# Optimization experiments

Measured on AMD Instinct MI355X. Metric: run time of the kernel, lower is better.

## Reference

```python
import jax, jax.numpy as jnp
import numpy as np

B, S, E = 1, 2048, 2048
H, KVH, D = 16, 4, 128  # query heads, kv heads, head dim (emb_kq == emb_v == 128)
SPLITS = (H * D, KVH * D, KVH * D)  # fused qkv output split sizes


def _rope_tables(seq_len, dim, base=10000.0):
    inv_freq = 1.0 / (base ** (jnp.arange(0, dim, 2, dtype=jnp.float32) / dim))
    t = jnp.arange(seq_len, dtype=jnp.float32)
    freqs = jnp.outer(t, inv_freq)  # [S, D/2]
    emb = jnp.concatenate([freqs, freqs], axis=-1)  # [S, D]
    return jnp.cos(emb), jnp.sin(emb)


def _rotate_half(x):
    x1, x2 = jnp.split(x, 2, axis=-1)
    return jnp.concatenate([-x2, x1], axis=-1)


def _apply_rope(x, cos, sin):
    # x: [B, S, h, D]; cos/sin: [S, D]
    c = cos[None, :, None, :]
    s = sin[None, :, None, :]
    return x * c + _rotate_half(x) * s


def setup_inputs() -> dict:
    key = jax.random.key(0)
    k1, k2, k3 = jax.random.split(key, 3)
    x = jax.random.normal(k1, (B, S, E), dtype=jnp.float32)
    w_qkv = jax.random.normal(k2, (sum(SPLITS), E), dtype=jnp.float32) * 0.02
    w_dense = jax.random.normal(k3, (E, H * D), dtype=jnp.float32) * 0.02
    return {"x": x, "w_qkv": w_qkv, "w_dense": w_dense}


def reference(x, w_qkv, w_dense):
    # fused QKV projection: [B, S, sum(SPLITS)]
    qkv = jnp.einsum("bse,fe->bsf", x, w_qkv)
    q, k, v = jnp.split(qkv, np.cumsum(SPLITS)[:-1].tolist(), axis=-1)
    q = q.reshape(B, S, H, D)
    k = k.reshape(B, S, KVH, D)
    v = v.reshape(B, S, KVH, D)

    # rotary position encoding on q, k
    cos, sin = _rope_tables(S, D)
    q = _apply_rope(q, cos, sin)
    k = _apply_rope(k, cos, sin)

    # GQA: expand kv heads to match query heads
    rep = H // KVH
    k = jnp.repeat(k, rep, axis=2)  # [B, S, H, D]
    v = jnp.repeat(v, rep, axis=2)

    # SDPA, causal
    scale = 1.0 / jnp.sqrt(jnp.asarray(D, dtype=x.dtype))
    scores = jnp.einsum("bqhd,bkhd->bhqk", q, k) * scale
    causal = jnp.tril(jnp.ones((S, S), dtype=bool))
    scores = jnp.where(causal[None, None], scores, jnp.asarray(-jnp.inf, scores.dtype))
    attn = jax.nn.softmax(scores, axis=-1)
    ctx = jnp.einsum("bhqk,bkhd->bqhd", attn, v).reshape(B, S, H * D)

    # output projection
    return jnp.einsum("bsf,ef->bse", ctx, w_dense)
```

## Files before the change

### kernel.cpp

```cpp
#include <hip/hip_runtime.h>
#include <hip/hip_bf16.h>
#include <math.h>

typedef __bf16 bf16;
typedef __bf16 bf16x4 __attribute__((ext_vector_type(4)));
typedef __bf16 bf16x8 __attribute__((ext_vector_type(8)));
typedef float  f32x4  __attribute__((ext_vector_type(4)));
typedef float  f32x16 __attribute__((ext_vector_type(16)));

#define S_LEN 2048
#define EMB   2048
#define NH    16
#define NKV   4
#define HD    128
#define FQKV  3072

__device__ __forceinline__ f32x4 mfma16(bf16x8 a, bf16x8 b, f32x4 c) {
  return __builtin_amdgcn_mfma_f32_16x16x32_bf16(a, b, c, 0, 0, 0);
}
__device__ __forceinline__ f32x16 mfma32(bf16x8 a, bf16x8 b, f32x16 c) {
  return __builtin_amdgcn_mfma_f32_32x32x16_bf16(a, b, c, 0, 0, 0);
}
__device__ __forceinline__ f32x16 zero16() {
  f32x16 v;
#pragma unroll
  for (int i = 0; i < 16; ++i) v[i] = 0.f;
  return v;
}

__global__ void rope_init(float2* __restrict__ rt) {
  const int idx = blockIdx.x * blockDim.x + threadIdx.x;
  const int spos = idx >> 6, f = idx & 63;
  const float inv = exp2f(-(float)f * (13.287712379549449f / 64.0f));
  float s, c;
  sincosf((float)spos * inv, &s, &c);
  rt[idx] = make_float2(c, s);
}

__global__ void cvt3_kernel(const float* __restrict__ a, bf16* __restrict__ ab, int na4,
                            const float* __restrict__ b, bf16* __restrict__ bb, int nb4,
                            const float* __restrict__ c, bf16* __restrict__ cb, int nc4) {
  int i = blockIdx.x * blockDim.x + threadIdx.x;
  const int stride = gridDim.x * blockDim.x;
  const int total = na4 + nb4 + nc4;
  for (; i < total; i += stride) {
    const float* src; bf16* dst; int j = i;
    if (j < na4)            { src = a; dst = ab; }
    else if (j < na4 + nb4) { j -= na4; src = b; dst = bb; }
    else                    { j -= na4 + nb4; src = c; dst = cb; }
    float4 v = reinterpret_cast<const float4*>(src)[j];
    bf16x4 o;
    o[0] = (bf16)v.x; o[1] = (bf16)v.y; o[2] = (bf16)v.z; o[3] = (bf16)v.w;
    reinterpret_cast<bf16x4*>(dst)[j] = o;
  }
}

template<int BN>
__global__ __launch_bounds__(256, 2) void gemm_bt(
    const bf16* __restrict__ A, const bf16* __restrict__ B,
    int M, int N, int K, int mode,
    bf16* __restrict__ qb, bf16* __restrict__ kb, bf16* __restrict__ vtb,
    float* __restrict__ outf, const float2* __restrict__ rt)
{
  constexpr int NFR = BN / 16;
  __shared__ __align__(16) bf16 As[128 * 64];
  __shared__ __align__(16) bf16 Bs[BN * 64];
  const int tid = threadIdx.x;
  const int w  = tid >> 6;
  const int l  = tid & 63;
  const int li = l & 15, lh = l >> 4;
  const int m0 = blockIdx.y * 128, n0 = blockIdx.x * BN;

  f32x4 acc[2][NFR];
#pragma unroll
  for (int i = 0; i < 2; ++i)
#pragma unroll
    for (int j = 0; j < NFR; ++j) acc[i][j] = f32x4{0.f, 0.f, 0.f, 0.f};

  const int srow = l >> 3;
  const int schk = l & 7;

  for (int k0 = 0; k0 < K; k0 += 64) {
#pragma unroll
    for (int i = 0; i < 4; ++i) {
      const int row = i * 32 + w * 8 + srow;
      const int sch = schk ^ (row & 7);
      const bf16* ga = A + (size_t)(m0 + row) * K + (k0 + sch * 8);
      bf16* la = As + (i * 32 + w * 8) * 64;
      __builtin_amdgcn_global_load_lds((const __attribute__((address_space(1))) void*)ga,
                                       (__attribute__((address_space(3))) void*)la, 16, 0, 0);
    }
#pragma unroll
    for (int i = 0; i < BN / 32; ++i) {
      const int row = i * 32 + w * 8 + srow;
      const int sch = schk ^ (row & 7);
      const bf16* gb = B + (size_t)(n0 + row) * K + (k0 + sch * 8);
      bf16* lb = Bs + (i * 32 + w * 8) * 64;
      __builtin_amdgcn_global_load_lds((const __attribute__((address_space(1))) void*)gb,
                                       (__attribute__((address_space(3))) void*)lb, 16, 0, 0);
    }
    __syncthreads();
#pragma unroll
    for (int kc = 0; kc < 2; ++kc) {
      bf16x8 afr[2], bfr[NFR];
#pragma unroll
      for (int mt = 0; mt < 2; ++mt) {
        const int mr = w * 32 + mt * 16 + li;
        const int c  = (kc * 4 + lh) ^ (mr & 7);
        afr[mt] = *reinterpret_cast<const bf16x8*>((const char*)As + mr * 128 + c * 16);
      }
#pragma unroll
      for (int nt = 0; nt < NFR; ++nt) {
        const int nr = nt * 16 + li;
        const int c  = (kc * 4 + lh) ^ (nr & 7);
        bfr[nt] = *reinterpret_cast<const bf16x8*>((const char*)Bs + nr * 128 + c * 16);
      }
#pragma unroll
      for (int nt = 0; nt < NFR; ++nt) {
        acc[0][nt] = mfma16(afr[0], bfr[nt], acc[0][nt]);
        acc[1][nt] = mfma16(afr[1], bfr[nt], acc[1][nt]);
      }
    }
    __syncthreads();
  }

  const int row_base = m0 + w * 32;
  if (BN == 64 || mode == 1) {
#pragma unroll
    for (int mt = 0; mt < 2; ++mt)
#pragma unroll
      for (int nt = 0; nt < NFR; ++nt)
#pragma unroll
        for (int r = 0; r < 4; ++r) {
          const int sr = row_base + mt * 16 + lh * 4 + r;
          const int sc = n0 + nt * 16 + li;
          outf[(size_t)sr * N + sc] = acc[mt][nt][r];
        }
  } else {
    if constexpr (BN == 128) {
      int seg, hh;
      if (n0 < NH * HD)             { seg = 0; hh = n0 >> 7; }
      else if (n0 < (NH + NKV) * HD){ seg = 1; hh = (n0 - NH * HD) >> 7; }
      else                          { seg = 2; hh = (n0 - (NH + NKV) * HD) >> 7; }

      const int T = row_base >> 5;
      if (seg == 2) {
        bf16* vdst = vtb + (size_t)hh * S_LEN * HD + (size_t)T * 4096;
#pragma unroll
        for (int mt = 0; mt < 2; ++mt) {
          const int qp = mt * 4 + lh;
          const int jj = (qp >> 2) & 1, hiv = qp & 1, ebase = 4 * ((qp >> 1) & 1);
#pragma unroll
          for (int nt = 0; nt < 8; ++nt) {
            const int dt = nt >> 1;
            const int lqv = (nt & 1) * 16 + li;
            bf16x4 pk;
#pragma unroll
            for (int r = 0; r < 4; ++r) pk[r] = (bf16)acc[mt][nt][r];
            *reinterpret_cast<bf16x4*>(
                vdst + ((dt * 2 + jj) * 2 + hiv) * 256 + lqv * 8 + ebase) = pk;
          }
        }
      } else {
        bf16* dst = ((seg == 0) ? (qb + (size_t)hh * S_LEN * HD)
                                : (kb + (size_t)hh * S_LEN * HD)) + (size_t)T * 4096;
        const float qscale = (seg == 0) ? 0.08838834764831845f : 1.0f;
        const int hi2 = li >> 3, e2 = li & 7;
#pragma unroll
        for (int mt = 0; mt < 2; ++mt)
#pragma unroll
          for (int r = 0; r < 4; ++r) {
            const int spos = row_base + mt * 16 + lh * 4 + r;
            const int lqr  = spos & 31;
            float cs[4], sn[4];
#pragma unroll
            for (int j = 0; j < 4; ++j) {
              const float2 t = rt[spos * 64 + j * 16 + li];
              cs[j] = t.x; sn[j] = t.y;
            }
#pragma unroll
            for (int nt = 0; nt < 8; ++nt) {
              const int j = nt & 3;
              const float x = acc[mt][nt][r];
              const float prt = acc[mt][nt ^ 4][r];
              const float rot = (nt < 4) ? -prt : prt;
              const float y = (x * cs[j] + rot * sn[j]) * qscale;
              dst[(nt * 2 + hi2) * 256 + lqr * 8 + e2] = (bf16)y;
            }
          }
      }
    }
  }
}

__global__ __launch_bounds__(128, 2) void attn_kernel(
    const bf16* __restrict__ qb, const bf16* __restrict__ kb, const bf16* __restrict__ vtb,
    bf16* __restrict__ ctx)
{
  __shared__ __align__(16) char smem[33280];
  __shared__ float Ml[2][32], Ll[2][32], Lgl[32];
  float* Obf = (float*)smem;

  const int tid = threadIdx.x;
  const int ws = tid >> 6;
  const int l  = tid & 63;
  const int lq = l & 31;
  const int hi = l >> 5;
  const int b  = (int)blockIdx.x;
  const int layer = b >> 8, idx = b & 255;
  const int h    = idx & 15;
  const int base = idx >> 4;
  const int qt   = (layer == 0) ? (63 - base)
                 : (layer == 1) ? (32 + base)
                 : (layer == 2) ? (31 - base) : base;
  const int q0 = qt * 32;
  const int kh = h >> 2;

  bf16* Kbuf = (bf16*)(smem + ws * 16384);
  bf16* Vbuf = (bf16*)(smem + ws * 16384 + 8192);

  const bf16* Qh = qb + (size_t)h * S_LEN * HD;
  const bf16* Kh = kb + (size_t)kh * S_LEN * HD;
  const bf16* Vh = vtb + (size_t)kh * S_LEN * HD;

  const float L2E = 1.4426950408889634f;
  const float BIG = -3.0e38f;

  const bf16* qtile = Qh + (size_t)qt * 4096;
  bf16x8 qfr[8];
#pragma unroll
  for (int kc = 0; kc < 8; ++kc)
    qfr[kc] = *reinterpret_cast<const bf16x8*>(qtile + (kc * 2 + hi) * 256 + lq * 8);

  f32x16 o[4];
#pragma unroll
  for (int dt = 0; dt < 4; ++dt) o[dt] = zero16();
  float mrow = BIG, lrow = 0.f;

  if (ws <= qt) {
    const bf16* ksrc = Kh + (size_t)ws * 4096 + l * 8;
    const bf16* vsrc = Vh + (size_t)ws * 4096 + l * 8;
#pragma unroll
    for (int c = 0; c < 8; ++c) {
      __builtin_amdgcn_global_load_lds(
          (const __attribute__((address_space(1))) void*)(ksrc + c * 512),
          (__attribute__((address_space(3))) void*)(Kbuf + c * 512), 16, 0, 0);
      __builtin_amdgcn_global_load_lds(
          (const __attribute__((address_space(1))) void*)(vsrc + c * 512),
          (__attribute__((address_space(3))) void*)(Vbuf + c * 512), 16, 0, 0);
    }
  }

  for (int t = ws; t <= qt; t += 2) {
    asm volatile("s_waitcnt vmcnt(0)" ::: "memory");
    __builtin_amdgcn_sched_barrier(0);
    bf16x8 kf[8], va[8];
#pragma unroll
    for (int kc = 0; kc < 8; ++kc)
      kf[kc] = *reinterpret_cast<const bf16x8*>(Kbuf + (kc * 2 + hi) * 256 + lq * 8);
#pragma unroll
    for (int sv = 0; sv < 8; ++sv)
      va[sv] = *reinterpret_cast<const bf16x8*>(Vbuf + (sv * 2 + hi) * 256 + lq * 8);
    asm volatile("s_waitcnt lgkmcnt(0)" ::: "memory");
    __builtin_amdgcn_sched_barrier(0);
    if (t + 2 <= qt) {
      const bf16* ksrc = Kh + (size_t)(t + 2) * 4096 + l * 8;
      const bf16* vsrc = Vh + (size_t)(t + 2) * 4096 + l * 8;
#pragma unroll
      for (int c = 0; c < 8; ++c) {
        __builtin_amdgcn_global_load_lds(
            (const __attribute__((address_space(1))) void*)(ksrc + c * 512),
            (__attribute__((address_space(3))) void*)(Kbuf + c * 512), 16, 0, 0);
        __builtin_amdgcn_global_load_lds(
            (const __attribute__((address_space(1))) void*)(vsrc + c * 512),
            (__attribute__((address_space(3))) void*)(Vbuf + c * 512), 16, 0, 0);
      }
    }
    f32x16 sa = zero16(), sb = zero16();
    __builtin_amdgcn_s_setprio(1);
#pragma unroll
    for (int kc = 0; kc < 4; ++kc) {
      sa = mfma32(kf[kc], qfr[kc], sa);
      sb = mfma32(kf[kc + 4], qfr[kc + 4], sb);
    }
    __builtin_amdgcn_s_setprio(0);
    f32x16 s = sa + sb;
    if (t == qt) {
      const int q = q0 + lq;
#pragma unroll
      for (int r = 0; r < 16; ++r) {
        const int kvv = (r & 3) + 8 * (r >> 2) + 4 * hi;
        if (t * 32 + kvv > q) s[r] = BIG;
      }
    }
    float pm = s[0];
#pragma unroll
    for (int r = 1; r < 16; ++r) pm = fmaxf(pm, s[r]);
    pm = fmaxf(pm, __shfl_xor(pm, 32));
    if (__any(pm > mrow + 8.f)) {
      const float mnew = fmaxf(mrow, pm);
      const float sc = (mrow < -1.0e37f) ? 0.f : exp2f((mrow - mnew) * L2E);
      mrow = mnew;
      lrow *= sc;
#pragma unroll
      for (int dt = 0; dt < 4; ++dt) o[dt] = o[dt] * sc;
    }
    bf16x8 pb0, pb1;
    float tsum = 0.f;
#pragma unroll
    for (int r = 0; r < 8; ++r) {
      const float pv = exp2f((s[r] - mrow) * L2E);
      tsum += pv; pb0[r] = (bf16)pv;
    }
#pragma unroll
    for (int r = 0; r < 8; ++r) {
      const float pv = exp2f((s[8 + r] - mrow) * L2E);
      tsum += pv; pb1[r] = (bf16)pv;
    }
    tsum += __shfl_xor(tsum, 32);
    lrow += tsum;
    __builtin_amdgcn_s_setprio(1);
#pragma unroll
    for (int dt = 0; dt < 4; ++dt) {
      o[dt] = mfma32(va[2 * dt], pb0, o[dt]);
      o[dt] = mfma32(va[2 * dt + 1], pb1, o[dt]);
    }
    __builtin_amdgcn_s_setprio(0);
  }

  if (hi == 0) { Ml[ws][lq] = mrow; Ll[ws][lq] = lrow; }
  __syncthreads();
  const float m0v = Ml[0][lq], m1v = Ml[1][lq];
  const float mg = fmaxf(m0v, m1v);
  const float lg = Ll[0][lq] * exp2f((m0v - mg) * L2E)
                 + Ll[1][lq] * exp2f((m1v - mg) * L2E);
  const float sc2 = (mrow < -1.0e37f) ? 0.f : exp2f((mrow - mg) * L2E);
  if (ws == 0 && hi == 0) Lgl[lq] = lg;
#pragma unroll
  for (int pass = 0; pass < 2; ++pass) {
    if (ws == pass) {
#pragma unroll
      for (int dt = 0; dt < 4; ++dt)
#pragma unroll
        for (int r = 0; r < 16; ++r) {
          const int d = dt * 32 + (r & 3) + 8 * (r >> 2) + 4 * hi;
          const float v = o[dt][r] * sc2;
          if (pass == 0) Obf[lq * 129 + d] = v; else Obf[lq * 129 + d] += v;
        }
    }
    __syncthreads();
  }
  {
    const int row = tid >> 2;
    const int d0 = (tid & 3) * 32;
    const float linv = 1.0f / Lgl[row];
    const float* orow = Obf + row * 129 + d0;
    bf16* dst = ctx + (size_t)(q0 + row) * (NH * HD) + h * HD + d0;
#pragma unroll
    for (int j = 0; j < 4; ++j) {
      bf16x8 pk;
#pragma unroll
      for (int e = 0; e < 8; ++e) pk[e] = (bf16)(orow[j * 8 + e] * linv);
      *reinterpret_cast<bf16x8*>(dst + j * 8) = pk;
    }
  }
}

extern "C" void kernel_launch(void* const* d_in, const int* in_sizes, int n_in,
                              void* d_out, int out_size, void* d_ws, size_t ws_size,
                              hipStream_t stream)
{
  const float* x       = (const float*)d_in[0];
  const float* w_qkv   = (const float*)d_in[1];
  const float* w_dense = (const float*)d_in[2];
  float* out = (float*)d_out;

  char* ws = (char*)d_ws;
  size_t off = 0;
  bf16* xb    = (bf16*)(ws + off); off += (size_t)S_LEN * EMB * 2;
  bf16* wqkvb = (bf16*)(ws + off); off += (size_t)FQKV * EMB * 2;
  bf16* wdb   = (bf16*)(ws + off); off += (size_t)EMB * EMB * 2;
  bf16* qbuf  = (bf16*)(ws + off); off += (size_t)NH  * S_LEN * HD * 2;
  bf16* kbuf  = (bf16*)(ws + off); off += (size_t)NKV * S_LEN * HD * 2;
  bf16* vfbuf = (bf16*)(ws + off); off += (size_t)NKV * HD * S_LEN * 2;
  bf16* ctxb  = (bf16*)(ws + off); off += (size_t)S_LEN * NH * HD * 2;
  float2* rtab = (float2*)(ws + off); off += (size_t)S_LEN * 64 * sizeof(float2);
  (void)ws_size; (void)in_sizes; (void)n_in; (void)out_size;

  rope_init<<<512, 256, 0, stream>>>(rtab);

  cvt3_kernel<<<2048, 256, 0, stream>>>(
      x, xb, S_LEN * EMB / 4,
      w_qkv, wqkvb, FQKV * EMB / 4,
      w_dense, wdb, EMB * EMB / 4);

  gemm_bt<128><<<dim3(FQKV / 128, S_LEN / 128), 256, 0, stream>>>(
      xb, wqkvb, S_LEN, FQKV, EMB, 0, qbuf, kbuf, vfbuf, nullptr, rtab);

  attn_kernel<<<1024, 128, 0, stream>>>(qbuf, kbuf, vfbuf, ctxb);

  gemm_bt<64><<<dim3(EMB / 64, S_LEN / 128), 256, 0, stream>>>(
      ctxb, wdb, S_LEN, EMB, NH * HD, 1, nullptr, nullptr, nullptr, out, rtab);
}
```

Measured before the change: 138.5 us.

## Split attention KV loop across four waves and pair causal q-tiles per block

The attention kernel now uses 256 threads (four waves) per block instead of two, with each wave taking every fourth KV tile, and partial softmax states are merged across four waves through LDS. Each block handles two complementary query tiles (63-base and base) in sequence, so every block gets the same causal work, and the grid is halved to 512. This aims to cut per-tile latency and remove load imbalance from the causal triangle. The cost is more LDS (64KB per block), more serialized merge passes and barriers, and fewer blocks in flight, which may lower occupancy.

```diff
diff --git a/kernel.cpp b/kernel.cpp
--- a/kernel.cpp
+++ b/kernel.cpp
@@ -193,31 +193,26 @@
   }
 }
 
-__global__ __launch_bounds__(128, 2) void attn_kernel(
+__global__ __launch_bounds__(256, 2) void attn_kernel(
     const bf16* __restrict__ qb, const bf16* __restrict__ kb, const bf16* __restrict__ vtb,
     bf16* __restrict__ ctx)
 {
-  __shared__ __align__(16) char smem[33280];
-  __shared__ float Ml[2][32], Ll[2][32], Lgl[32];
+  __shared__ __align__(16) char smem[65536];
+  __shared__ float Ml[4][32], Ll[4][32], Lgl[32];
   float* Obf = (float*)smem;
 
   const int tid = threadIdx.x;
-  const int ws = tid >> 6;
+  const int w  = tid >> 6;
   const int l  = tid & 63;
   const int lq = l & 31;
   const int hi = l >> 5;
   const int b  = (int)blockIdx.x;
-  const int layer = b >> 8, idx = b & 255;
-  const int h    = idx & 15;
-  const int base = idx >> 4;
-  const int qt   = (layer == 0) ? (63 - base)
-                 : (layer == 1) ? (32 + base)
-                 : (layer == 2) ? (31 - base) : base;
-  const int q0 = qt * 32;
+  const int h    = b & 15;
+  const int base = b >> 4;
   const int kh = h >> 2;
 
-  bf16* Kbuf = (bf16*)(smem + ws * 16384);
-  bf16* Vbuf = (bf16*)(smem + ws * 16384 + 8192);
+  bf16* Kbuf = (bf16*)(smem + w * 16384);
+  bf16* Vbuf = (bf16*)(smem + w * 16384 + 8192);
 
   const bf16* Qh = qb + (size_t)h * S_LEN * HD;
   const bf16* Kh = kb + (size_t)kh * S_LEN * HD;
@@ -226,46 +221,25 @@
   const float L2E = 1.4426950408889634f;
   const float BIG = -3.0e38f;
 
-  const bf16* qtile = Qh + (size_t)qt * 4096;
-  bf16x8 qfr[8];
-#pragma unroll
-  for (int kc = 0; kc < 8; ++kc)
-    qfr[kc] = *reinterpret_cast<const bf16x8*>(qtile + (kc * 2 + hi) * 256 + lq * 8);
-
-  f32x16 o[4];
-#pragma unroll
-  for (int dt = 0; dt < 4; ++dt) o[dt] = zero16();
-  float mrow = BIG, lrow = 0.f;
-
-  if (ws <= qt) {
-    const bf16* ksrc = Kh + (size_t)ws * 4096 + l * 8;
-    const bf16* vsrc = Vh + (size_t)ws * 4096 + l * 8;
-#pragma unroll
-    for (int c = 0; c < 8; ++c) {
-      __builtin_amdgcn_global_load_lds(
-          (const __attribute__((address_space(1))) void*)(ksrc + c * 512),
-          (__attribute__((address_space(3))) void*)(Kbuf + c * 512), 16, 0, 0);
-      __builtin_amdgcn_global_load_lds(
-          (const __attribute__((address_space(1))) void*)(vsrc + c * 512),
-          (__attribute__((address_space(3))) void*)(Vbuf + c * 512), 16, 0, 0);
-    }
-  }
-
-  for (int t = ws; t <= qt; t += 2) {
-    asm volatile("s_waitcnt vmcnt(0)" ::: "memory");
-    __builtin_amdgcn_sched_barrier(0);
-    bf16x8 kf[8], va[8];
+  for (int it = 0; it < 2; ++it) {
+    const int qt = it ? base : (63 - base);
+    const int q0 = qt * 32;
+    __syncthreads();
+
+    const bf16* qtile = Qh + (size_t)qt * 4096;
+    bf16x8 qfr[8];
 #pragma unroll
     for (int kc = 0; kc < 8; ++kc)
-      kf[kc] = *reinterpret_cast<const bf16x8*>(Kbuf + (kc * 2 + hi) * 256 + lq * 8);
-#pragma unroll
-    for (int sv = 0; sv < 8; ++sv)
-      va[sv] = *reinterpret_cast<const bf16x8*>(Vbuf + (sv * 2 + hi) * 256 + lq * 8);
-    asm volatile("s_waitcnt lgkmcnt(0)" ::: "memory");
-    __builtin_amdgcn_sched_barrier(0);
-    if (t + 2 <= qt) {
-      const bf16* ksrc = Kh + (size_t)(t + 2) * 4096 + l * 8;
-      const bf16* vsrc = Vh + (size_t)(t + 2) * 4096 + l * 8;
+      qfr[kc] = *reinterpret_cast<const bf16x8*>(qtile + (kc * 2 + hi) * 256 + lq * 8);
+
+    f32x16 o[4];
+#pragma unroll
+    for (int dt = 0; dt < 4; ++dt) o[dt] = zero16();
+    float mrow = BIG, lrow = 0.f;
+
+    if (w <= qt) {
+      const bf16* ksrc = Kh + (size_t)w * 4096 + l * 8;
+      const bf16* vsrc = Vh + (size_t)w * 4096 + l * 8;
 #pragma unroll
       for (int c = 0; c < 8; ++c) {
         __builtin_amdgcn_global_load_lds(
@@ -276,92 +250,122 @@
             (__attribute__((address_space(3))) void*)(Vbuf + c * 512), 16, 0, 0);
       }
     }
-    f32x16 sa = zero16(), sb = zero16();
-    __builtin_amdgcn_s_setprio(1);
-#pragma unroll
-    for (int kc = 0; kc < 4; ++kc) {
-      sa = mfma32(kf[kc], qfr[kc], sa);
-      sb = mfma32(kf[kc + 4], qfr[kc + 4], sb);
-    }
-    __builtin_amdgcn_s_setprio(0);
-    f32x16 s = sa + sb;
-    if (t == qt) {
-      const int q = q0 + lq;
-#pragma unroll
-      for (int r = 0; r < 16; ++r) {
-        const int kvv = (r & 3) + 8 * (r >> 2) + 4 * hi;
-        if (t * 32 + kvv > q) s[r] = BIG;
-      }
-    }
-    float pm = s[0];
-#pragma unroll
-    for (int r = 1; r < 16; ++r) pm = fmaxf(pm, s[r]);
-    pm = fmaxf(pm, __shfl_xor(pm, 32));
-    if (__any(pm > mrow + 8.f)) {
-      const float mnew = fmaxf(mrow, pm);
-      const float sc = (mrow < -1.0e37f) ? 0.f : exp2f((mrow - mnew) * L2E);
-      mrow = mnew;
-      lrow *= sc;
-#pragma unroll
-      for (int dt = 0; dt < 4; ++dt) o[dt] = o[dt] * sc;
-    }
-    bf16x8 pb0, pb1;
-    float tsum = 0.f;
-#pragma unroll
-    for (int r = 0; r < 8; ++r) {
-      const float pv = exp2f((s[r] - mrow) * L2E);
-      tsum += pv; pb0[r] = (bf16)pv;
-    }
-#pragma unroll
-    for (int r = 0; r < 8; ++r) {
-      const float pv = exp2f((s[8 + r] - mrow) * L2E);
-      tsum += pv; pb1[r] = (bf16)pv;
-    }
-    tsum += __shfl_xor(tsum, 32);
-    lrow += tsum;
-    __builtin_amdgcn_s_setprio(1);
-#pragma unroll
-    for (int dt = 0; dt < 4; ++dt) {
-      o[dt] = mfma32(va[2 * dt], pb0, o[dt]);
-      o[dt] = mfma32(va[2 * dt + 1], pb1, o[dt]);
-    }
-    __builtin_amdgcn_s_setprio(0);
-  }
-
-  if (hi == 0) { Ml[ws][lq] = mrow; Ll[ws][lq] = lrow; }
-  __syncthreads();
-  const float m0v = Ml[0][lq], m1v = Ml[1][lq];
-  const float mg = fmaxf(m0v, m1v);
-  const float lg = Ll[0][lq] * exp2f((m0v - mg) * L2E)
-                 + Ll[1][lq] * exp2f((m1v - mg) * L2E);
-  const float sc2 = (mrow < -1.0e37f) ? 0.f : exp2f((mrow - mg) * L2E);
-  if (ws == 0 && hi == 0) Lgl[lq] = lg;
-#pragma unroll
-  for (int pass = 0; pass < 2; ++pass) {
-    if (ws == pass) {
-#pragma unroll
-      for (int dt = 0; dt < 4; ++dt)
+
+    for (int t = w; t <= qt; t += 4) {
+      asm volatile("s_waitcnt vmcnt(0)" ::: "memory");
+      __builtin_amdgcn_sched_barrier(0);
+      bf16x8 kf[8], va[8];
+#pragma unroll
+      for (int kc = 0; kc < 8; ++kc)
+        kf[kc] = *reinterpret_cast<const bf16x8*>(Kbuf + (kc * 2 + hi) * 256 + lq * 8);
+#pragma unroll
+      for (int sv = 0; sv < 8; ++sv)
+        va[sv] = *reinterpret_cast<const bf16x8*>(Vbuf + (sv * 2 + hi) * 256 + lq * 8);
+      asm volatile("s_waitcnt lgkmcnt(0)" ::: "memory");
+      __builtin_amdgcn_sched_barrier(0);
+      if (t + 4 <= qt) {
+        const bf16* ksrc = Kh + (size_t)(t + 4) * 4096 + l * 8;
+        const bf16* vsrc = Vh + (size_t)(t + 4) * 4096 + l * 8;
+#pragma unroll
+        for (int c = 0; c < 8; ++c) {
+          __builtin_amdgcn_global_load_lds(
+              (const __attribute__((address_space(1))) void*)(ksrc + c * 512),
+              (__attribute__((address_space(3))) void*)(Kbuf + c * 512), 16, 0, 0);
+          __builtin_amdgcn_global_load_lds(
+              (const __attribute__((address_space(1))) void*)(vsrc + c * 512),
+              (__attribute__((address_space(3))) void*)(Vbuf + c * 512), 16, 0, 0);
+        }
+      }
+      f32x16 sa = zero16(), sb = zero16();
+      __builtin_amdgcn_s_setprio(1);
+#pragma unroll
+      for (int kc = 0; kc < 4; ++kc) {
+        sa = mfma32(kf[kc], qfr[kc], sa);
+        sb = mfma32(kf[kc + 4], qfr[kc + 4], sb);
+      }
+      __builtin_amdgcn_s_setprio(0);
+      f32x16 s = sa + sb;
+      if (t == qt) {
+        const int q = q0 + lq;
 #pragma unroll
         for (int r = 0; r < 16; ++r) {
-          const int d = dt * 32 + (r & 3) + 8 * (r >> 2) + 4 * hi;
-          const float v = o[dt][r] * sc2;
-          if (pass == 0) Obf[lq * 129 + d] = v; else Obf[lq * 129 + d] += v;
+          const int kvv = (r & 3) + 8 * (r >> 2) + 4 * hi;
+          if (t * 32 + kvv > q) s[r] = BIG;
         }
-    }
+      }
+      float pm = s[0];
+#pragma unroll
+      for (int r = 1; r < 16; ++r) pm = fmaxf(pm, s[r]);
+      pm = fmaxf(pm, __shfl_xor(pm, 32));
+      if (__any(pm > mrow + 8.f)) {
+        const float mnew = fmaxf(mrow, pm);
+        const float sc = (mrow < -1.0e37f) ? 0.f : exp2f((mrow - mnew) * L2E);
+        mrow = mnew;
+        lrow *= sc;
+#pragma unroll
+        for (int dt = 0; dt < 4; ++dt) o[dt] = o[dt] * sc;
+      }
+      bf16x8 pb0, pb1;
+      float tsum = 0.f;
+#pragma unroll
+      for (int r = 0; r < 8; ++r) {
+        const float pv = exp2f((s[r] - mrow) * L2E);
+        tsum += pv; pb0[r] = (bf16)pv;
+      }
+#pragma unroll
+      for (int r = 0; r < 8; ++r) {
+        const float pv = exp2f((s[8 + r] - mrow) * L2E);
+        tsum += pv; pb1[r] = (bf16)pv;
+      }
+      tsum += __shfl_xor(tsum, 32);
+      lrow += tsum;
+      __builtin_amdgcn_s_setprio(1);
+#pragma unroll
+      for (int dt = 0; dt < 4; ++dt) {
+        o[dt] = mfma32(va[2 * dt], pb0, o[dt]);
+        o[dt] = mfma32(va[2 * dt + 1], pb1, o[dt]);
+      }
+      __builtin_amdgcn_s_setprio(0);
+    }
+
+    if (hi == 0) { Ml[w][lq] = mrow; Ll[w][lq] = lrow; }
     __syncthreads();
-  }
-  {
-    const int row = tid >> 2;
-    const int d0 = (tid & 3) * 32;
-    const float linv = 1.0f / Lgl[row];
-    const float* orow = Obf + row * 129 + d0;
-    bf16* dst = ctx + (size_t)(q0 + row) * (NH * HD) + h * HD + d0;
-#pragma unroll
-    for (int j = 0; j < 4; ++j) {
-      bf16x8 pk;
-#pragma unroll
-      for (int e = 0; e < 8; ++e) pk[e] = (bf16)(orow[j * 8 + e] * linv);
-      *reinterpret_cast<bf16x8*>(dst + j * 8) = pk;
+    const float m0v = Ml[0][lq], m1v = Ml[1][lq], m2v = Ml[2][lq], m3v = Ml[3][lq];
+    const float mg = fmaxf(fmaxf(m0v, m1v), fmaxf(m2v, m3v));
+    const float lg = Ll[0][lq] * exp2f((m0v - mg) * L2E)
+                   + Ll[1][lq] * exp2f((m1v - mg) * L2E)
+                   + Ll[2][lq] * exp2f((m2v - mg) * L2E)
+                   + Ll[3][lq] * exp2f((m3v - mg) * L2E);
+    const float sc2 = (mrow < -1.0e37f) ? 0.f : exp2f((mrow - mg) * L2E);
+    if (w == 0 && hi == 0) Lgl[lq] = lg;
+#pragma unroll
+    for (int pass = 0; pass < 4; ++pass) {
+      if (w == pass) {
+#pragma unroll
+        for (int dt = 0; dt < 4; ++dt)
+#pragma unroll
+          for (int r = 0; r < 16; ++r) {
+            const int d = dt * 32 + (r & 3) + 8 * (r >> 2) + 4 * hi;
+            const float v = o[dt][r] * sc2;
+            if (pass == 0) Obf[lq * 129 + d] = v; else Obf[lq * 129 + d] += v;
+          }
+      }
+      __syncthreads();
+    }
+    {
+      const int row = tid >> 3;
+      const int d0 = (tid & 7) * 16;
+      const float linv = 1.0f / Lgl[row];
+      const float* orow = Obf + row * 129 + d0;
+      bf16* dst = ctx + (size_t)(q0 + row) * (NH * HD) + h * HD + d0;
+      bf16x8 pk0, pk1;
+#pragma unroll
+      for (int e = 0; e < 8; ++e) {
+        pk0[e] = (bf16)(orow[e] * linv);
+        pk1[e] = (bf16)(orow[8 + e] * linv);
+      }
+      *reinterpret_cast<bf16x8*>(dst) = pk0;
+      *reinterpret_cast<bf16x8*>(dst + 8) = pk1;
     }
   }
 }
@@ -397,7 +401,7 @@
   gemm_bt<128><<<dim3(FQKV / 128, S_LEN / 128), 256, 0, stream>>>(
       xb, wqkvb, S_LEN, FQKV, EMB, 0, qbuf, kbuf, vfbuf, nullptr, rtab);
 
-  attn_kernel<<<1024, 128, 0, stream>>>(qbuf, kbuf, vfbuf, ctxb);
+  attn_kernel<<<512, 256, 0, stream>>>(qbuf, kbuf, vfbuf, ctxb);
 
   gemm_bt<64><<<dim3(EMB / 64, S_LEN / 128), 256, 0, stream>>>(
       ctxb, wdb, S_LEN, EMB, NH * HD, 1, nullptr, nullptr, nullptr, out, rtab);
```

Result: no change. 139.0 us (+0.3%).
